# Optimization experiments

Measured on AMD Instinct MI355X. Metric: run time of the kernel, lower is better.

Reference implementation:

```python
import jax, jax.numpy as jnp
import numpy as np

B, T, V = 32, 64, 30000
EMB, H, E, A = 512, 512, 256, 256


def setup_inputs() -> dict:
    key = jax.random.key(0)
    ks = jax.random.split(key, 16)
    s = lambda k, shape, fan: jax.random.normal(k, shape, jnp.float32) / np.sqrt(fan)
    return {
        "encoder_out": jax.random.normal(ks[0], (B, E), jnp.float32),
        "captions": jax.random.randint(ks[1], (B, T), 0, V),
        # attention params
        "We": s(ks[2], (A, E), E), "be": jnp.zeros((A,), jnp.float32),
        "Wd": s(ks[3], (A, H), H), "bd": jnp.zeros((A,), jnp.float32),
        "Wf": s(ks[4], (1, A), A), "bf": jnp.zeros((1,), jnp.float32),
        # embedding table
        "emb_table": s(ks[5], (V, EMB), 1.0),
        # LSTMCell params (PyTorch gate order i,f,g,o)
        "W_ih": s(ks[6], (4 * H, EMB + E), EMB + E),
        "W_hh": s(ks[7], (4 * H, H), H),
        "b_ih": jnp.zeros((4 * H,), jnp.float32),
        "b_hh": jnp.zeros((4 * H,), jnp.float32),
        # output projection
        "W_fc": s(ks[8], (V, H), H), "b_fc": jnp.zeros((V,), jnp.float32),
    }


def reference(encoder_out, captions, We, be, Wd, bd, Wf, bf, emb_table,
              W_ih, W_hh, b_ih, b_hh, W_fc, b_fc):
    # dropout layers are identity (eval mode)
    emb = emb_table[captions]                      # [B, T, EMB]
    att1 = encoder_out @ We.T + be                 # [B, A]  (encoder term, loop-invariant)

    def step(carry, e_t):
        h, c = carry
        # additive attention over a length-1 sequence -> alpha == 1
        att2 = h @ Wd.T + bd                       # [B, A]
        att = jnp.tanh(att1 + att2) @ Wf.T + bf    # [B, 1]
        alpha = jax.nn.softmax(att, axis=1)        # ones, kept for faithfulness
        context = encoder_out * alpha              # [B, E]
        x = jnp.concatenate([e_t, context], axis=1)  # [B, EMB+E]
        gates = x @ W_ih.T + b_ih + h @ W_hh.T + b_hh  # [B, 4H]
        i, f, g, o = jnp.split(gates, 4, axis=1)
        c_new = jax.nn.sigmoid(f) * c + jax.nn.sigmoid(i) * jnp.tanh(g)
        h_new = jax.nn.sigmoid(o) * jnp.tanh(c_new)
        out_t = h_new @ W_fc.T + b_fc              # [B, V]
        return (h_new, c_new), out_t

    h0 = jnp.zeros((encoder_out.shape[0], H), encoder_out.dtype)
    c0 = jnp.zeros_like(h0)
    _, outs = jax.lax.scan(step, (h0, c0), jnp.swapaxes(emb, 0, 1))  # [T, B, V]
    return jnp.swapaxes(outs, 0, 1)                                  # [B, T, V]
```

## Files before the change

### kernel.cpp

```cpp
#include <hip/hip_runtime.h>
#include <hip/hip_bf16.h>


#define BATCH 32
#define TT 64
#define VV 30000
#define HH 512
#define G4 2048
#define KX 768
#define RNN_WG 16

typedef __bf16 bf16x8 __attribute__((ext_vector_type(8)));
typedef float f32x4 __attribute__((ext_vector_type(4)));
typedef __attribute__((address_space(1))) void gvoid;
typedef __attribute__((address_space(3))) void lvoid;

#define MFMA(a, b, c) __builtin_amdgcn_mfma_f32_16x16x32_bf16((a), (b), (c), 0, 0, 0)

__device__ __forceinline__ float sigf(float x) {
    return 1.0f / (1.0f + __expf(-x));
}
__device__ __forceinline__ float tanh_fast(float x) {
    return 1.0f - 2.0f / (__expf(2.0f * x) + 1.0f);
}
__device__ __forceinline__ bf16x8 cvt8(const float* __restrict__ p) {
    const f32x4 a = *(const f32x4*)p;
    const f32x4 b = *(const f32x4*)(p + 4);
    bf16x8 r;
    r[0] = (__bf16)a[0]; r[1] = (__bf16)a[1]; r[2] = (__bf16)a[2]; r[3] = (__bf16)a[3];
    r[4] = (__bf16)b[0]; r[5] = (__bf16)b[1]; r[6] = (__bf16)b[2]; r[7] = (__bf16)b[3];
    return r;
}

__global__ __launch_bounds__(256) void pre_kernel(
    const float* __restrict__ enc, const int* __restrict__ captions,
    const float* __restrict__ emb, const float* __restrict__ Wih,
    const float* __restrict__ bih, const float* __restrict__ bhh,
    float* __restrict__ pre) {
    __shared__ __bf16 aT[128 * 32];
    __shared__ __bf16 bT[128 * 32];
    __shared__ int capm[128];

    const int tid = threadIdx.x;
    const int nt = blockIdx.x;
    const int mt = blockIdx.y;

    if (tid < 128) {
        int m = mt * 128 + tid;
        capm[tid] = captions[(m & 31) * TT + (m >> 5)];
    }

    const int lane = tid & 63, wv = tid >> 6;
    const int ln = lane & 15, quad = lane >> 4;
    const int wm = wv & 1, wn = wv >> 1;

    f32x4 acc[4][4] = {};
    __syncthreads();

    for (int kc = 0; kc < 24; ++kc) {
        const int k0 = kc * 32;
        for (int i = tid; i < 512; i += 256) {
            int r = i >> 2, seg = i & 3;
            const float* src;
            if (k0 < 512) {
                src = emb + (size_t)capm[r] * 512 + k0 + seg * 8;
            } else {
                int b = (mt * 128 + r) & 31;
                src = enc + b * 256 + (k0 - 512) + seg * 8;
            }
            *(bf16x8*)&aT[r * 32 + seg * 8] = cvt8(src);
            *(bf16x8*)&bT[r * 32 + seg * 8] =
                cvt8(&Wih[(size_t)(nt * 128 + r) * KX + k0 + seg * 8]);
        }
        __syncthreads();
        bf16x8 af[4], bfr[4];
        for (int x = 0; x < 4; ++x) {
            af[x]  = *(const bf16x8*)&aT[(wm * 64 + x * 16 + ln) * 32 + quad * 8];
            bfr[x] = *(const bf16x8*)&bT[(wn * 64 + x * 16 + ln) * 32 + quad * 8];
        }
        for (int mi = 0; mi < 4; ++mi)
            for (int ni = 0; ni < 4; ++ni)
                acc[mi][ni] = MFMA(af[mi], bfr[ni], acc[mi][ni]);
        __syncthreads();
    }

    for (int ni = 0; ni < 4; ++ni) {
        int g = nt * 128 + wn * 64 + ni * 16 + ln;
        float bias = bih[g] + bhh[g];
        for (int mi = 0; mi < 4; ++mi) {
            int m = mt * 128 + wm * 64 + mi * 16 + quad * 4;
            int t = m >> 5, b = m & 31;
            f32x4 v = acc[mi][ni];
            v[0] += bias; v[1] += bias; v[2] += bias; v[3] += bias;
            *(f32x4*)&pre[((size_t)t * G4 + g) * BATCH + b] = v;
        }
    }
}

__global__ __launch_bounds__(256, 1) void rnn_kernel(
    const float* __restrict__ pre, const float* __restrict__ Whh,
    __bf16* __restrict__ Hall, unsigned* __restrict__ flags,
    const float* __restrict__ Wfc, __bf16* __restrict__ Wfc16) {
    __shared__ char smem[131072];

    if (blockIdx.x >= RNN_WG) {
        if (Wfc16) {
            const int stride = (gridDim.x - RNN_WG) * 256;
            int idx = (blockIdx.x - RNN_WG) * 256 + threadIdx.x;
            for (int i = idx; i < VV * HH / 8; i += stride)
                *(bf16x8*)&Wfc16[(size_t)i * 8] = cvt8(&Wfc[(size_t)i * 8]);
        }
        return;
    }

    __bf16* whh = (__bf16*)smem;
    float*  gst = (float*)smem;

    const int tid = threadIdx.x;
    const int w = blockIdx.x;
    const int lane = tid & 63, wv = tid >> 6;
    const int ln = lane & 15, quad = lane >> 4;

    for (int i = tid; i < 128 * 64; i += 256) {
        int r = i >> 6, k = (i & 63) << 3;
        int g = (r >> 5) * 512 + w * 32 + (r & 31);
        *(bf16x8*)&whh[r * 512 + k] = cvt8(&Whh[(size_t)g * HH + k]);
    }
    __syncthreads();

    bf16x8 bfrag[2][16];
#pragma unroll
    for (int nj = 0; nj < 2; ++nj)
#pragma unroll
        for (int kc = 0; kc < 16; ++kc)
            bfrag[nj][kc] = *(const bf16x8*)
                &whh[(wv * 32 + nj * 16 + ln) * 512 + kc * 32 + quad * 8];
    __syncthreads();

    const int b_pw = tid & 31;
    const int nl = tid >> 5;
    const int b0 = quad * 4;
    const size_t preg0 = (size_t)(wv * 512 + w * 32 + ln);
    float c[4] = {0.f, 0.f, 0.f, 0.f};

    for (int t = 0; t < TT; ++t) {
        f32x4 acc[2][2];
#pragma unroll
        for (int mi = 0; mi < 2; ++mi)
#pragma unroll
            for (int nj = 0; nj < 2; ++nj)
                acc[mi][nj] = *(const f32x4*)
                    &pre[((size_t)t * G4 + preg0 + nj * 16) * BATCH + mi * 16 + b0];

        if (t > 0) {
            if (tid < RNN_WG) {
                while (__hip_atomic_load(&flags[(t - 1) * RNN_WG + tid],
                                         __ATOMIC_RELAXED,
                                         __HIP_MEMORY_SCOPE_AGENT) == 0) {}
            }
        }
        __syncthreads();

        if (t > 0) {
            const __bf16* hbase = Hall + (size_t)(t - 1) * BATCH * HH;
            bf16x8 a[2][8];
#pragma unroll
            for (int half = 0; half < 2; ++half) {
#pragma unroll
                for (int mi = 0; mi < 2; ++mi)
#pragma unroll
                    for (int kk = 0; kk < 8; ++kk)
                        a[mi][kk] = *(const bf16x8*)
                            &hbase[(size_t)(mi * 16 + ln) * HH +
                                   (half * 8 + kk) * 32 + quad * 8];
#pragma unroll
                for (int kk = 0; kk < 8; ++kk)
#pragma unroll
                    for (int mi = 0; mi < 2; ++mi)
#pragma unroll
                        for (int nj = 0; nj < 2; ++nj)
                            acc[mi][nj] = MFMA(a[mi][kk],
                                               bfrag[nj][half * 8 + kk],
                                               acc[mi][nj]);
            }
        }
#pragma unroll
        for (int mi = 0; mi < 2; ++mi)
#pragma unroll
            for (int nj = 0; nj < 2; ++nj)
                *(f32x4*)&gst[(wv * 32 + nj * 16 + ln) * 36 + mi * 16 + b0] =
                    acc[mi][nj];
        __syncthreads();

        union { unsigned long long u; __bf16 h4[4]; } pk;
#pragma unroll
        for (int j = 0; j < 4; ++j) {
            int cl = nl * 4 + j;
            float gi = gst[(cl)      * 36 + b_pw];
            float gf = gst[(32 + cl) * 36 + b_pw];
            float gg = gst[(64 + cl) * 36 + b_pw];
            float go = gst[(96 + cl) * 36 + b_pw];
            c[j] = sigf(gf) * c[j] + sigf(gi) * tanh_fast(gg);
            pk.h4[j] = (__bf16)(sigf(go) * tanh_fast(c[j]));
        }
        __hip_atomic_store(
            (unsigned long long*)&Hall[((size_t)t * BATCH + b_pw) * HH +
                                       w * 32 + nl * 4],
            pk.u, __ATOMIC_RELAXED, __HIP_MEMORY_SCOPE_AGENT);

        __syncthreads();
        if (tid == 0 && t < TT - 1)
            __hip_atomic_store(&flags[t * RNN_WG + w], 1u, __ATOMIC_RELAXED,
                               __HIP_MEMORY_SCOPE_AGENT);
    }
}

template <int BF16W>
__global__ __launch_bounds__(256) void out_kernel(
    const __bf16* __restrict__ Hall, const float* __restrict__ Wfc,
    const __bf16* __restrict__ Wfc16, const float* __restrict__ bfc,
    float* __restrict__ out) {
    __shared__ __bf16 aT[128 * 32];
    __shared__ __bf16 bT[128 * 32];

    const int tid = threadIdx.x;
    const int mt = blockIdx.x;
    const int nt = blockIdx.y;
    const int lane = tid & 63, wv = tid >> 6;
    const int ln = lane & 15, quad = lane >> 4;
    const int wm = wv & 1, wn = wv >> 1;

    f32x4 acc[4][4] = {};
    const size_t aBase = (size_t)mt * 128 * HH;

    for (int kc = 0; kc < 16; ++kc) {
        const int k0 = kc * 32;
        if (BF16W) {
#pragma unroll
            for (int h = 0; h < 2; ++h) {
                int ch = tid + h * 256;
                int r = ch >> 2, seg = ch & 3;
                const __bf16* asrc = &Hall[aBase + (size_t)r * HH + k0 + seg * 8];
                int gr = nt * 128 + r;
                if (gr >= VV) gr = VV - 1;
                const __bf16* bsrc = &Wfc16[(size_t)gr * HH + k0 + seg * 8];
                __builtin_amdgcn_global_load_lds(
                    (gvoid*)asrc,
                    (lvoid*)((char*)aT + wv * 1024 + h * 4096), 16, 0, 0);
                __builtin_amdgcn_global_load_lds(
                    (gvoid*)bsrc,
                    (lvoid*)((char*)bT + wv * 1024 + h * 4096), 16, 0, 0);
            }
        } else {
            for (int i = tid; i < 512; i += 256) {
                int r = i >> 2, seg = i & 3;
                *(bf16x8*)&aT[r * 32 + seg * 8] =
                    *(const bf16x8*)&Hall[aBase + (size_t)r * HH + k0 + seg * 8];
                int gr = nt * 128 + r;
                if (gr >= VV) gr = VV - 1;
                *(bf16x8*)&bT[r * 32 + seg * 8] =
                    cvt8(&Wfc[(size_t)gr * HH + k0 + seg * 8]);
            }
        }
        __syncthreads();
        bf16x8 af[4], bfr[4];
        for (int x = 0; x < 4; ++x) {
            af[x]  = *(const bf16x8*)&aT[(wm * 64 + x * 16 + ln) * 32 + quad * 8];
            bfr[x] = *(const bf16x8*)&bT[(wn * 64 + x * 16 + ln) * 32 + quad * 8];
        }
        for (int mi = 0; mi < 4; ++mi)
            for (int ni = 0; ni < 4; ++ni)
                acc[mi][ni] = MFMA(af[mi], bfr[ni], acc[mi][ni]);
        __syncthreads();
    }

    for (int ni = 0; ni < 4; ++ni) {
        int n = nt * 128 + wn * 64 + ni * 16 + ln;
        if (n >= VV) continue;
        float bias = bfc[n];
        for (int mi = 0; mi < 4; ++mi) {
            int m = mt * 128 + wm * 64 + mi * 16 + quad * 4;
            for (int r = 0; r < 4; ++r) {
                int mm = m + r, t = mm >> 5, b = mm & 31;
                out[((size_t)b * TT + t) * VV + n] = acc[mi][ni][r] + bias;
            }
        }
    }
}

extern "C" void kernel_launch(void* const* d_in, const int* in_sizes, int n_in,
                              void* d_out, int out_size, void* d_ws, size_t ws_size,
                              hipStream_t stream) {
    const float* enc      = (const float*)d_in[0];
    const int*   captions = (const int*)d_in[1];
    const float* emb      = (const float*)d_in[8];
    const float* Wih      = (const float*)d_in[9];
    const float* Whh      = (const float*)d_in[10];
    const float* bih      = (const float*)d_in[11];
    const float* bhh      = (const float*)d_in[12];
    const float* Wfc      = (const float*)d_in[13];
    const float* bfc      = (const float*)d_in[14];
    float* out = (float*)d_out;

    float* pre = (float*)d_out;

    uint8_t* w = (uint8_t*)d_ws;
    unsigned* flags = (unsigned*)w;
    __bf16*   Hall  = (__bf16*)(w + 16384);
    const size_t WFC16_OFF = 16384 + (size_t)TT * BATCH * HH * 2;
    const bool bf16w = ws_size >= WFC16_OFF + (size_t)VV * HH * 2;
    __bf16* Wfc16 = bf16w ? (__bf16*)(w + WFC16_OFF) : (__bf16*)nullptr;

    hipMemsetAsync(flags, 0, 16384, stream);

    pre_kernel<<<dim3(16, 16), 256, 0, stream>>>(enc, captions, emb, Wih, bih, bhh, pre);
    rnn_kernel<<<dim3(256), 256, 0, stream>>>(pre, Whh, Hall, flags, Wfc, Wfc16);
    if (bf16w)
        out_kernel<1><<<dim3(16, 235), 256, 0, stream>>>(Hall, Wfc, Wfc16, bfc, out);
    else
        out_kernel<0><<<dim3(16, 235), 256, 0, stream>>>(Hall, Wfc, Wfc16, bfc, out);
}
```

Measured before the change: 951.1 us.

## Replace flag barrier with poison-sentinel dataflow polling on hidden state

Removes the per-step flag array and the block barrier plus flag store that signalled completion. The hidden-state buffer is pre-filled with an all-ones poison pattern, and consumers poll the h values directly, running the MFMAs for each K-chunk as soon as it arrives. The pre-activation load for the next step is also prefetched into registers. This cuts a global round trip and a barrier per timestep, at the cost of more atomic loads, higher register pressure, and reliance on 64-bit stores being atomic and on real values never matching the poison pattern.

New measurement: 1.158 ms. 1.22x slower.

```diff
diff --git a/kernel.cpp b/kernel.cpp
--- a/kernel.cpp
+++ b/kernel.cpp
@@ -14,6 +14,9 @@
 typedef float f32x4 __attribute__((ext_vector_type(4)));
 typedef __attribute__((address_space(1))) void gvoid;
 typedef __attribute__((address_space(3))) void lvoid;
+typedef unsigned long long u64;
+
+#define POISON 0xFFFFFFFFFFFFFFFFull
 
 #define MFMA(a, b, c) __builtin_amdgcn_mfma_f32_16x16x32_bf16((a), (b), (c), 0, 0, 0)
 
@@ -30,6 +33,10 @@
     r[0] = (__bf16)a[0]; r[1] = (__bf16)a[1]; r[2] = (__bf16)a[2]; r[3] = (__bf16)a[3];
     r[4] = (__bf16)b[0]; r[5] = (__bf16)b[1]; r[6] = (__bf16)b[2]; r[7] = (__bf16)b[3];
     return r;
+}
+__device__ __forceinline__ u64 aload(const __bf16* p) {
+    return __hip_atomic_load((const u64*)p, __ATOMIC_RELAXED,
+                             __HIP_MEMORY_SCOPE_AGENT);
 }
 
 __global__ __launch_bounds__(256) void pre_kernel(
@@ -99,7 +106,7 @@
 
 __global__ __launch_bounds__(256, 1) void rnn_kernel(
     const float* __restrict__ pre, const float* __restrict__ Whh,
-    __bf16* __restrict__ Hall, unsigned* __restrict__ flags,
+    __bf16* __restrict__ Hall,
     const float* __restrict__ Wfc, __bf16* __restrict__ Wfc16) {
     __shared__ char smem[131072];
 
@@ -143,47 +150,87 @@
     const size_t preg0 = (size_t)(wv * 512 + w * 32 + ln);
     float c[4] = {0.f, 0.f, 0.f, 0.f};
 
+    f32x4 pr[2][2];
+#pragma unroll
+    for (int mi = 0; mi < 2; ++mi)
+#pragma unroll
+        for (int nj = 0; nj < 2; ++nj)
+            pr[mi][nj] = *(const f32x4*)
+                &pre[((size_t)0 * G4 + preg0 + nj * 16) * BATCH + mi * 16 + b0];
+
     for (int t = 0; t < TT; ++t) {
         f32x4 acc[2][2];
 #pragma unroll
         for (int mi = 0; mi < 2; ++mi)
 #pragma unroll
             for (int nj = 0; nj < 2; ++nj)
-                acc[mi][nj] = *(const f32x4*)
-                    &pre[((size_t)t * G4 + preg0 + nj * 16) * BATCH + mi * 16 + b0];
-
+                acc[mi][nj] = pr[mi][nj];
+
+        u64 d[16][2][2];
+        const __bf16* hb = Hall + (size_t)(t - 1) * BATCH * HH;
         if (t > 0) {
-            if (tid < RNN_WG) {
-                while (__hip_atomic_load(&flags[(t - 1) * RNN_WG + tid],
-                                         __ATOMIC_RELAXED,
-                                         __HIP_MEMORY_SCOPE_AGENT) == 0) {}
-            }
-        }
-        __syncthreads();
+#pragma unroll
+            for (int kc = 0; kc < 16; ++kc)
+#pragma unroll
+                for (int mi = 0; mi < 2; ++mi) {
+                    const __bf16* p =
+                        hb + (size_t)(mi * 16 + ln) * HH + kc * 32 + quad * 8;
+                    d[kc][mi][0] = aload(p);
+                    d[kc][mi][1] = aload(p + 4);
+                }
+        }
+
+        if (t + 1 < TT) {
+#pragma unroll
+            for (int mi = 0; mi < 2; ++mi)
+#pragma unroll
+                for (int nj = 0; nj < 2; ++nj)
+                    pr[mi][nj] = *(const f32x4*)
+                        &pre[((size_t)(t + 1) * G4 + preg0 + nj * 16) * BATCH +
+                             mi * 16 + b0];
+        }
 
         if (t > 0) {
-            const __bf16* hbase = Hall + (size_t)(t - 1) * BATCH * HH;
-            bf16x8 a[2][8];
-#pragma unroll
-            for (int half = 0; half < 2; ++half) {
-#pragma unroll
-                for (int mi = 0; mi < 2; ++mi)
-#pragma unroll
-                    for (int kk = 0; kk < 8; ++kk)
-                        a[mi][kk] = *(const bf16x8*)
-                            &hbase[(size_t)(mi * 16 + ln) * HH +
-                                   (half * 8 + kk) * 32 + quad * 8];
-#pragma unroll
-                for (int kk = 0; kk < 8; ++kk)
-#pragma unroll
-                    for (int mi = 0; mi < 2; ++mi)
-#pragma unroll
-                        for (int nj = 0; nj < 2; ++nj)
-                            acc[mi][nj] = MFMA(a[mi][kk],
-                                               bfrag[nj][half * 8 + kk],
-                                               acc[mi][nj]);
-            }
-        }
+            unsigned pend = 0xFFFFu;
+            while (pend) {
+#pragma unroll
+                for (int kc = 0; kc < 16; ++kc) {
+                    if (pend & (1u << kc)) {
+                        bool cl = (d[kc][0][0] != POISON) &
+                                  (d[kc][0][1] != POISON) &
+                                  (d[kc][1][0] != POISON) &
+                                  (d[kc][1][1] != POISON);
+                        if (__all(cl)) {
+                            union { u64 q[2]; bf16x8 v; } u0, u1;
+                            u0.q[0] = d[kc][0][0]; u0.q[1] = d[kc][0][1];
+                            u1.q[0] = d[kc][1][0]; u1.q[1] = d[kc][1][1];
+                            acc[0][0] = MFMA(u0.v, bfrag[0][kc], acc[0][0]);
+                            acc[0][1] = MFMA(u0.v, bfrag[1][kc], acc[0][1]);
+                            acc[1][0] = MFMA(u1.v, bfrag[0][kc], acc[1][0]);
+                            acc[1][1] = MFMA(u1.v, bfrag[1][kc], acc[1][1]);
+                            pend &= ~(1u << kc);
+                        }
+                    }
+                }
+                if (pend) {
+#pragma unroll
+                    for (int kc = 0; kc < 16; ++kc) {
+                        if (pend & (1u << kc)) {
+#pragma unroll
+                            for (int mi = 0; mi < 2; ++mi) {
+                                const __bf16* p = hb +
+                                    (size_t)(mi * 16 + ln) * HH + kc * 32 +
+                                    quad * 8;
+                                d[kc][mi][0] = aload(p);
+                                d[kc][mi][1] = aload(p + 4);
+                            }
+                        }
+                    }
+                }
+            }
+        }
+
+        __syncthreads();
 #pragma unroll
         for (int mi = 0; mi < 2; ++mi)
 #pragma unroll
@@ -192,7 +239,7 @@
                     acc[mi][nj];
         __syncthreads();
 
-        union { unsigned long long u; __bf16 h4[4]; } pk;
+        union { u64 u; __bf16 h4[4]; } pk;
 #pragma unroll
         for (int j = 0; j < 4; ++j) {
             int cl = nl * 4 + j;
@@ -204,14 +251,8 @@
             pk.h4[j] = (__bf16)(sigf(go) * tanh_fast(c[j]));
         }
         __hip_atomic_store(
-            (unsigned long long*)&Hall[((size_t)t * BATCH + b_pw) * HH +
-                                       w * 32 + nl * 4],
+            (u64*)&Hall[((size_t)t * BATCH + b_pw) * HH + w * 32 + nl * 4],
             pk.u, __ATOMIC_RELAXED, __HIP_MEMORY_SCOPE_AGENT);
-
-        __syncthreads();
-        if (tid == 0 && t < TT - 1)
-            __hip_atomic_store(&flags[t * RNN_WG + w], 1u, __ATOMIC_RELAXED,
-                               __HIP_MEMORY_SCOPE_AGENT);
     }
 }
 
@@ -305,16 +346,15 @@
     float* pre = (float*)d_out;
 
     uint8_t* w = (uint8_t*)d_ws;
-    unsigned* flags = (unsigned*)w;
-    __bf16*   Hall  = (__bf16*)(w + 16384);
-    const size_t WFC16_OFF = 16384 + (size_t)TT * BATCH * HH * 2;
-    const bool bf16w = ws_size >= WFC16_OFF + (size_t)VV * HH * 2;
-    __bf16* Wfc16 = bf16w ? (__bf16*)(w + WFC16_OFF) : (__bf16*)nullptr;
-
-    hipMemsetAsync(flags, 0, 16384, stream);
+    __bf16* Hall = (__bf16*)w;
+    const size_t HALL_BYTES = (size_t)TT * BATCH * HH * 2;
+    const bool bf16w = ws_size >= HALL_BYTES + (size_t)VV * HH * 2;
+    __bf16* Wfc16 = bf16w ? (__bf16*)(w + HALL_BYTES) : (__bf16*)nullptr;
+
+    hipMemsetAsync(Hall, 0xFF, HALL_BYTES, stream);
 
     pre_kernel<<<dim3(16, 16), 256, 0, stream>>>(enc, captions, emb, Wih, bih, bhh, pre);
-    rnn_kernel<<<dim3(256), 256, 0, stream>>>(pre, Whh, Hall, flags, Wfc, Wfc16);
+    rnn_kernel<<<dim3(256), 256, 0, stream>>>(pre, Whh, Hall, Wfc, Wfc16);
     if (bf16w)
         out_kernel<1><<<dim3(16, 235), 256, 0, stream>>>(Hall, Wfc, Wfc16, bfc, out);
     else
```

## Fuse output projection into persistent RNN kernel with flag-gated consumer blocks

Applied to the files above, without the earlier changes.

The output-projection GEMM now runs inside the recurrent kernel. The 240 non-recurrent blocks wait on per-timestep flags and compute 128-row output tiles as soon as the four timesteps feeding each tile are finished, so the projection overlaps the serial recurrence. The pre-activation buffer moves into workspace so the consumers can write the output directly. The bf16 copy of W_fc is dropped, so consumers convert fp32 weights on the fly, and the per-step pre-activation load is software-prefetched one step ahead. The costs are extra fp32 weight traffic, spin-waiting blocks that may contend with the recurrent blocks, and a dependence on the workspace being large enough.

Measured after the change: 868.8 us. -8.7%, faster.

```diff
diff --git a/kernel.cpp b/kernel.cpp
--- a/kernel.cpp
+++ b/kernel.cpp
@@ -9,11 +9,12 @@
 #define G4 2048
 #define KX 768
 #define RNN_WG 16
+#define CONS_WG 240
+#define NTILE 235
 
 typedef __bf16 bf16x8 __attribute__((ext_vector_type(8)));
 typedef float f32x4 __attribute__((ext_vector_type(4)));
-typedef __attribute__((address_space(1))) void gvoid;
-typedef __attribute__((address_space(3))) void lvoid;
+typedef unsigned long long u64;
 
 #define MFMA(a, b, c) __builtin_amdgcn_mfma_f32_16x16x32_bf16((a), (b), (c), 0, 0, 0)
 
@@ -97,29 +98,77 @@
     }
 }
 
-__global__ __launch_bounds__(256, 1) void rnn_kernel(
+__global__ __launch_bounds__(256, 1) void fused_kernel(
     const float* __restrict__ pre, const float* __restrict__ Whh,
     __bf16* __restrict__ Hall, unsigned* __restrict__ flags,
-    const float* __restrict__ Wfc, __bf16* __restrict__ Wfc16) {
+    const float* __restrict__ Wfc, const float* __restrict__ bfc,
+    float* __restrict__ out, int consume) {
     __shared__ char smem[131072];
+    const int tid = threadIdx.x;
+    const int lane = tid & 63, wv = tid >> 6;
+    const int ln = lane & 15, quad = lane >> 4;
 
     if (blockIdx.x >= RNN_WG) {
-        if (Wfc16) {
-            const int stride = (gridDim.x - RNN_WG) * 256;
-            int idx = (blockIdx.x - RNN_WG) * 256 + threadIdx.x;
-            for (int i = idx; i < VV * HH / 8; i += stride)
-                *(bf16x8*)&Wfc16[(size_t)i * 8] = cvt8(&Wfc[(size_t)i * 8]);
+        if (!consume) return;
+        __bf16* aT = (__bf16*)smem;
+        __bf16* bT = (__bf16*)(smem + 8192);
+        const int wm = wv & 1, wn = wv >> 1;
+        const int cw = blockIdx.x - RNN_WG;
+
+        for (int j = cw; j < 16 * NTILE; j += CONS_WG) {
+            const int mt = j / NTILE, nt = j % NTILE;
+            if (tid < RNN_WG) {
+                const unsigned fidx = (unsigned)(mt * 4 + 3) * RNN_WG + tid;
+                while (__hip_atomic_load(&flags[fidx], __ATOMIC_RELAXED,
+                                         __HIP_MEMORY_SCOPE_AGENT) == 0)
+                    __builtin_amdgcn_s_sleep(2);
+            }
+            __syncthreads();
+
+            f32x4 acc[4][4] = {};
+            const size_t aBase = (size_t)mt * 128 * HH;
+            for (int kc = 0; kc < 16; ++kc) {
+                const int k0 = kc * 32;
+                for (int i = tid; i < 512; i += 256) {
+                    int r = i >> 2, seg = i & 3;
+                    *(bf16x8*)&aT[r * 32 + seg * 8] = *(const bf16x8*)
+                        &Hall[aBase + (size_t)r * HH + k0 + seg * 8];
+                    int gr = nt * 128 + r;
+                    if (gr >= VV) gr = VV - 1;
+                    *(bf16x8*)&bT[r * 32 + seg * 8] =
+                        cvt8(&Wfc[(size_t)gr * HH + k0 + seg * 8]);
+                }
+                __syncthreads();
+                bf16x8 af[4], bfr[4];
+                for (int x = 0; x < 4; ++x) {
+                    af[x]  = *(const bf16x8*)&aT[(wm * 64 + x * 16 + ln) * 32 + quad * 8];
+                    bfr[x] = *(const bf16x8*)&bT[(wn * 64 + x * 16 + ln) * 32 + quad * 8];
+                }
+                for (int mi = 0; mi < 4; ++mi)
+                    for (int ni = 0; ni < 4; ++ni)
+                        acc[mi][ni] = MFMA(af[mi], bfr[ni], acc[mi][ni]);
+                __syncthreads();
+            }
+
+            for (int ni = 0; ni < 4; ++ni) {
+                int n = nt * 128 + wn * 64 + ni * 16 + ln;
+                if (n >= VV) continue;
+                float bias = bfc[n];
+                for (int mi = 0; mi < 4; ++mi) {
+                    int m = mt * 128 + wm * 64 + mi * 16 + quad * 4;
+                    for (int r = 0; r < 4; ++r) {
+                        int mm = m + r, t = mm >> 5, b = mm & 31;
+                        out[((size_t)b * TT + t) * VV + n] = acc[mi][ni][r] + bias;
+                    }
+                }
+            }
         }
         return;
     }
 
     __bf16* whh = (__bf16*)smem;
     float*  gst = (float*)smem;
-
-    const int tid = threadIdx.x;
     const int w = blockIdx.x;
-    const int lane = tid & 63, wv = tid >> 6;
-    const int ln = lane & 15, quad = lane >> 4;
 
     for (int i = tid; i < 128 * 64; i += 256) {
         int r = i >> 6, k = (i & 63) << 3;
@@ -143,14 +192,31 @@
     const size_t preg0 = (size_t)(wv * 512 + w * 32 + ln);
     float c[4] = {0.f, 0.f, 0.f, 0.f};
 
+    f32x4 pr[2][2];
+#pragma unroll
+    for (int mi = 0; mi < 2; ++mi)
+#pragma unroll
+        for (int nj = 0; nj < 2; ++nj)
+            pr[mi][nj] = *(const f32x4*)
+                &pre[(preg0 + nj * 16) * BATCH + mi * 16 + b0];
+
     for (int t = 0; t < TT; ++t) {
         f32x4 acc[2][2];
 #pragma unroll
         for (int mi = 0; mi < 2; ++mi)
 #pragma unroll
             for (int nj = 0; nj < 2; ++nj)
-                acc[mi][nj] = *(const f32x4*)
-                    &pre[((size_t)t * G4 + preg0 + nj * 16) * BATCH + mi * 16 + b0];
+                acc[mi][nj] = pr[mi][nj];
+
+        if (t + 1 < TT) {
+#pragma unroll
+            for (int mi = 0; mi < 2; ++mi)
+#pragma unroll
+                for (int nj = 0; nj < 2; ++nj)
+                    pr[mi][nj] = *(const f32x4*)
+                        &pre[((size_t)(t + 1) * G4 + preg0 + nj * 16) * BATCH +
+                             mi * 16 + b0];
+        }
 
         if (t > 0) {
             if (tid < RNN_WG) {
@@ -192,7 +258,7 @@
                     acc[mi][nj];
         __syncthreads();
 
-        union { unsigned long long u; __bf16 h4[4]; } pk;
+        union { u64 u; __bf16 h4[4]; } pk;
 #pragma unroll
         for (int j = 0; j < 4; ++j) {
             int cl = nl * 4 + j;
@@ -204,22 +270,19 @@
             pk.h4[j] = (__bf16)(sigf(go) * tanh_fast(c[j]));
         }
         __hip_atomic_store(
-            (unsigned long long*)&Hall[((size_t)t * BATCH + b_pw) * HH +
-                                       w * 32 + nl * 4],
+            (u64*)&Hall[((size_t)t * BATCH + b_pw) * HH + w * 32 + nl * 4],
             pk.u, __ATOMIC_RELAXED, __HIP_MEMORY_SCOPE_AGENT);
 
         __syncthreads();
-        if (tid == 0 && t < TT - 1)
+        if (tid == 0)
             __hip_atomic_store(&flags[t * RNN_WG + w], 1u, __ATOMIC_RELAXED,
                                __HIP_MEMORY_SCOPE_AGENT);
     }
 }
 
-template <int BF16W>
 __global__ __launch_bounds__(256) void out_kernel(
     const __bf16* __restrict__ Hall, const float* __restrict__ Wfc,
-    const __bf16* __restrict__ Wfc16, const float* __restrict__ bfc,
-    float* __restrict__ out) {
+    const float* __restrict__ bfc, float* __restrict__ out) {
     __shared__ __bf16 aT[128 * 32];
     __shared__ __bf16 bT[128 * 32];
 
@@ -235,32 +298,14 @@
 
     for (int kc = 0; kc < 16; ++kc) {
         const int k0 = kc * 32;
-        if (BF16W) {
-#pragma unroll
-            for (int h = 0; h < 2; ++h) {
-                int ch = tid + h * 256;
-                int r = ch >> 2, seg = ch & 3;
-                const __bf16* asrc = &Hall[aBase + (size_t)r * HH + k0 + seg * 8];
-                int gr = nt * 128 + r;
-                if (gr >= VV) gr = VV - 1;
-                const __bf16* bsrc = &Wfc16[(size_t)gr * HH + k0 + seg * 8];
-                __builtin_amdgcn_global_load_lds(
-                    (gvoid*)asrc,
-                    (lvoid*)((char*)aT + wv * 1024 + h * 4096), 16, 0, 0);
-                __builtin_amdgcn_global_load_lds(
-                    (gvoid*)bsrc,
-                    (lvoid*)((char*)bT + wv * 1024 + h * 4096), 16, 0, 0);
-            }
-        } else {
-            for (int i = tid; i < 512; i += 256) {
-                int r = i >> 2, seg = i & 3;
-                *(bf16x8*)&aT[r * 32 + seg * 8] =
-                    *(const bf16x8*)&Hall[aBase + (size_t)r * HH + k0 + seg * 8];
-                int gr = nt * 128 + r;
-                if (gr >= VV) gr = VV - 1;
-                *(bf16x8*)&bT[r * 32 + seg * 8] =
-                    cvt8(&Wfc[(size_t)gr * HH + k0 + seg * 8]);
-            }
+        for (int i = tid; i < 512; i += 256) {
+            int r = i >> 2, seg = i & 3;
+            *(bf16x8*)&aT[r * 32 + seg * 8] =
+                *(const bf16x8*)&Hall[aBase + (size_t)r * HH + k0 + seg * 8];
+            int gr = nt * 128 + r;
+            if (gr >= VV) gr = VV - 1;
+            *(bf16x8*)&bT[r * 32 + seg * 8] =
+                cvt8(&Wfc[(size_t)gr * HH + k0 + seg * 8]);
         }
         __syncthreads();
         bf16x8 af[4], bfr[4];
@@ -302,21 +347,20 @@
     const float* bfc      = (const float*)d_in[14];
     float* out = (float*)d_out;
 
-    float* pre = (float*)d_out;
-
     uint8_t* w = (uint8_t*)d_ws;
     unsigned* flags = (unsigned*)w;
-    __bf16*   Hall  = (__bf16*)(w + 16384);
-    const size_t WFC16_OFF = 16384 + (size_t)TT * BATCH * HH * 2;
-    const bool bf16w = ws_size >= WFC16_OFF + (size_t)VV * HH * 2;
-    __bf16* Wfc16 = bf16w ? (__bf16*)(w + WFC16_OFF) : (__bf16*)nullptr;
+    __bf16* Hall = (__bf16*)(w + 16384);
+    const size_t PRE_OFF   = 16384 + (size_t)TT * BATCH * HH * 2;
+    const size_t PRE_BYTES = (size_t)TT * G4 * BATCH * 4;
+    const bool fused = ws_size >= PRE_OFF + PRE_BYTES;
+
+    float* pre = fused ? (float*)(w + PRE_OFF) : (float*)d_out;
 
     hipMemsetAsync(flags, 0, 16384, stream);
 
     pre_kernel<<<dim3(16, 16), 256, 0, stream>>>(enc, captions, emb, Wih, bih, bhh, pre);
-    rnn_kernel<<<dim3(256), 256, 0, stream>>>(pre, Whh, Hall, flags, Wfc, Wfc16);
-    if (bf16w)
-        out_kernel<1><<<dim3(16, 235), 256, 0, stream>>>(Hall, Wfc, Wfc16, bfc, out);
-    else
-        out_kernel<0><<<dim3(16, 235), 256, 0, stream>>>(Hall, Wfc, Wfc16, bfc, out);
-}
+    fused_kernel<<<dim3(256), 256, 0, stream>>>(pre, Whh, Hall, flags, Wfc, bfc,
+                                                out, fused ? 1 : 0);
+    if (!fused)
+        out_kernel<<<dim3(16, 235), 256, 0, stream>>>(Hall, Wfc, bfc, out);
+}
```
